# Kernel optimization log

Measured on AMD Instinct MI355X. Metric: run time of the kernel, lower is better.

## Reference

```python
import jax, jax.numpy as jnp
import numpy as np

B, N, C = 8, 32768, 4
M = 11          # memory_length
D = 5           # degree
K = D * M       # basis size per (channel, time) = M linear + (D-1)*M envelope terms


def setup_inputs() -> dict:
    key = jax.random.key(0)
    kx, kw = jax.random.split(key)
    x = jax.random.normal(kx, (B, N, C, 2), dtype=jnp.float32)
    # xavier-uniform over [C, K]
    limit = float(np.sqrt(6.0 / (C + K)))
    Weight = jax.random.uniform(kw, (C, K), minval=-limit, maxval=limit, dtype=jnp.float32)
    return {"x": x, "Weight": Weight}


def _windows(a, m):
    # a: [..., L] -> [..., L-m+1, m]; windows[..., n, j] = a[..., n+j]
    n_out = a.shape[-1] - m + 1
    return jnp.stack([a[..., j:j + n_out] for j in range(m)], axis=-1)


def reference(x, Weight):
    b, n, c, _ = x.shape
    # [B,N,C,2] -> complex [B,C,N]
    xc = (x[..., 0] + 1j * x[..., 1]).transpose(0, 2, 1)
    pad = jnp.zeros((b, c, M - 1), dtype=xc.dtype)
    padded = jnp.concatenate([pad, xc], axis=2)                 # [B,C,N+M-1]
    windows_x = _windows(padded, M)                             # [B,C,N,M] complex
    amp = jnp.abs(padded)                                       # [B,C,N+M-1]
    x_degree = jnp.stack([amp ** i for i in range(1, D)], axis=1)  # [B,D-1,C,L]
    windows_degree = _windows(x_degree, M)                      # [B,D-1,C,N,M]
    mul_term = windows_x[:, None] * windows_degree              # [B,D-1,C,N,M] complex
    mul_term = mul_term.transpose(0, 2, 3, 1, 4).reshape(b, c, n, (D - 1) * M)
    x_input = jnp.concatenate([windows_x, mul_term], axis=3)    # [B,C,N,D*M]
    out_c = jnp.einsum('bcnk,ck->bcn', x_input, Weight.astype(x_input.dtype))
    out_c = out_c.transpose(0, 2, 1)                            # [B,N,C]
    return jnp.stack([out_c.real, out_c.imag], axis=3)          # [B,N,C,2]
```

## Files before the change

### kernel.cpp

```cpp
#include <hip/hip_runtime.h>

#define BB 8
#define NN 32768
#define CC 4
#define MM 11
#define DD 5
#define KK 55
#define BLOCK_N 256
#define HALO (MM - 1)
#define SS (BLOCK_N + HALO)


__global__ __launch_bounds__(256, 4)
void gmp_kernel(const float* __restrict__ x,
                const float* __restrict__ W,
                float* __restrict__ out) {
    __shared__ float4 smem[SS * 3];

    const int tid = threadIdx.x;
    const int b = blockIdx.y;
    const int n0 = blockIdx.x * BLOCK_N;

    const float4* xg = (const float4*)x + (size_t)b * NN * 2;

    for (int s = tid; s < SS; s += BLOCK_N) {
        const int t = n0 - HALO + s;
        float4 lo = make_float4(0.f, 0.f, 0.f, 0.f);
        float4 hi = lo;
        if (t >= 0) {
            lo = xg[2 * t];
            hi = xg[2 * t + 1];
        }
        float4 a;
        a.x = sqrtf(fmaf(lo.x, lo.x, lo.y * lo.y));
        a.y = sqrtf(fmaf(lo.z, lo.z, lo.w * lo.w));
        a.z = sqrtf(fmaf(hi.x, hi.x, hi.y * hi.y));
        a.w = sqrtf(fmaf(hi.z, hi.z, hi.w * hi.w));
        smem[s * 3 + 0] = lo;
        smem[s * 3 + 1] = hi;
        smem[s * 3 + 2] = a;
    }
    __syncthreads();

    float acc_re[CC] = {0.f, 0.f, 0.f, 0.f};
    float acc_im[CC] = {0.f, 0.f, 0.f, 0.f};

    #pragma unroll
    for (int j = 0; j < MM; j++) {
        const int s = tid + j;
        const float4 lo = smem[s * 3 + 0];
        const float4 hi = smem[s * 3 + 1];
        const float4 a  = smem[s * 3 + 2];
        const float re[CC] = {lo.x, lo.z, hi.x, hi.z};
        const float im[CC] = {lo.y, lo.w, hi.y, hi.w};
        const float am[CC] = {a.x, a.y, a.z, a.w};
        #pragma unroll
        for (int c = 0; c < CC; c++) {
            float p = W[c * KK + 4 * MM + j];
            p = fmaf(p, am[c], W[c * KK + 3 * MM + j]);
            p = fmaf(p, am[c], W[c * KK + 2 * MM + j]);
            p = fmaf(p, am[c], W[c * KK + 1 * MM + j]);
            p = fmaf(p, am[c], W[c * KK + 0 * MM + j]);
            acc_re[c] = fmaf(re[c], p, acc_re[c]);
            acc_im[c] = fmaf(im[c], p, acc_im[c]);
        }
    }

    const int n = n0 + tid;
    float4* og = (float4*)out + (size_t)(b * NN + n) * 2;
    og[0] = make_float4(acc_re[0], acc_im[0], acc_re[1], acc_im[1]);
    og[1] = make_float4(acc_re[2], acc_im[2], acc_re[3], acc_im[3]);
}

extern "C" void kernel_launch(void* const* d_in, const int* in_sizes, int n_in,
                              void* d_out, int out_size, void* d_ws, size_t ws_size,
                              hipStream_t stream) {
    const float* x = (const float*)d_in[0];
    const float* W = (const float*)d_in[1];
    float* out = (float*)d_out;

    dim3 grid(NN / BLOCK_N, BB);
    gmp_kernel<<<grid, BLOCK_N, 0, stream>>>(x, W, out);
}
```

Measured before the change: 63.51 us.

## Split channel pairs across grid z-dimension to increase parallelism and occupancy

```diff
diff --git a/kernel.cpp b/kernel.cpp
--- a/kernel.cpp
+++ b/kernel.cpp
@@ -4,72 +4,71 @@
 #define NN 32768
 #define CC 4
 #define MM 11
-#define DD 5
 #define KK 55
-#define BLOCK_N 256
+#define THREADS 256
 #define HALO (MM - 1)
-#define SS (BLOCK_N + HALO)
+#define SS (THREADS + HALO)
 
 
-__global__ __launch_bounds__(256, 4)
+__global__ __launch_bounds__(THREADS, 8)
 void gmp_kernel(const float* __restrict__ x,
                 const float* __restrict__ W,
                 float* __restrict__ out) {
-    __shared__ float4 smem[SS * 3];
+    __shared__ float4 zs[SS];
+    __shared__ float2 as2[SS];
 
     const int tid = threadIdx.x;
-    const int b = blockIdx.y;
-    const int n0 = blockIdx.x * BLOCK_N;
+    const int b  = blockIdx.y;
+    const int h  = blockIdx.z;
+    const int n0 = blockIdx.x * THREADS;
 
     const float4* xg = (const float4*)x + (size_t)b * NN * 2;
 
-    for (int s = tid; s < SS; s += BLOCK_N) {
+    for (int s = tid; s < SS; s += THREADS) {
         const int t = n0 - HALO + s;
-        float4 lo = make_float4(0.f, 0.f, 0.f, 0.f);
-        float4 hi = lo;
-        if (t >= 0) {
-            lo = xg[2 * t];
-            hi = xg[2 * t + 1];
-        }
-        float4 a;
-        a.x = sqrtf(fmaf(lo.x, lo.x, lo.y * lo.y));
-        a.y = sqrtf(fmaf(lo.z, lo.z, lo.w * lo.w));
-        a.z = sqrtf(fmaf(hi.x, hi.x, hi.y * hi.y));
-        a.w = sqrtf(fmaf(hi.z, hi.z, hi.w * hi.w));
-        smem[s * 3 + 0] = lo;
-        smem[s * 3 + 1] = hi;
-        smem[s * 3 + 2] = a;
+        float4 v = make_float4(0.f, 0.f, 0.f, 0.f);
+        if (t >= 0) v = xg[2 * t + h];
+        float2 a;
+        a.x = sqrtf(fmaf(v.x, v.x, v.y * v.y));
+        a.y = sqrtf(fmaf(v.z, v.z, v.w * v.w));
+        zs[s] = v;
+        as2[s] = a;
     }
     __syncthreads();
 
-    float acc_re[CC] = {0.f, 0.f, 0.f, 0.f};
-    float acc_im[CC] = {0.f, 0.f, 0.f, 0.f};
+    const float* W0 = W + (2 * h) * KK;
+    const float* W1 = W + (2 * h + 1) * KK;
+
+    float ar0 = 0.f, ai0 = 0.f, ar1 = 0.f, ai1 = 0.f;
 
     #pragma unroll
     for (int j = 0; j < MM; j++) {
         const int s = tid + j;
-        const float4 lo = smem[s * 3 + 0];
-        const float4 hi = smem[s * 3 + 1];
-        const float4 a  = smem[s * 3 + 2];
-        const float re[CC] = {lo.x, lo.z, hi.x, hi.z};
-        const float im[CC] = {lo.y, lo.w, hi.y, hi.w};
-        const float am[CC] = {a.x, a.y, a.z, a.w};
-        #pragma unroll
-        for (int c = 0; c < CC; c++) {
-            float p = W[c * KK + 4 * MM + j];
-            p = fmaf(p, am[c], W[c * KK + 3 * MM + j]);
-            p = fmaf(p, am[c], W[c * KK + 2 * MM + j]);
-            p = fmaf(p, am[c], W[c * KK + 1 * MM + j]);
-            p = fmaf(p, am[c], W[c * KK + 0 * MM + j]);
-            acc_re[c] = fmaf(re[c], p, acc_re[c]);
-            acc_im[c] = fmaf(im[c], p, acc_im[c]);
+        const float4 v = zs[s];
+        const float2 a = as2[s];
+        {
+            float p = W0[4 * MM + j];
+            p = fmaf(p, a.x, W0[3 * MM + j]);
+            p = fmaf(p, a.x, W0[2 * MM + j]);
+            p = fmaf(p, a.x, W0[1 * MM + j]);
+            p = fmaf(p, a.x, W0[0 * MM + j]);
+            ar0 = fmaf(v.x, p, ar0);
+            ai0 = fmaf(v.y, p, ai0);
+        }
+        {
+            float p = W1[4 * MM + j];
+            p = fmaf(p, a.y, W1[3 * MM + j]);
+            p = fmaf(p, a.y, W1[2 * MM + j]);
+            p = fmaf(p, a.y, W1[1 * MM + j]);
+            p = fmaf(p, a.y, W1[0 * MM + j]);
+            ar1 = fmaf(v.z, p, ar1);
+            ai1 = fmaf(v.w, p, ai1);
         }
     }
 
     const int n = n0 + tid;
-    float4* og = (float4*)out + (size_t)(b * NN + n) * 2;
-    og[0] = make_float4(acc_re[0], acc_im[0], acc_re[1], acc_im[1]);
-    og[1] = make_float4(acc_re[2], acc_im[2], acc_re[3], acc_im[3]);
+    float4* og = (float4*)out + ((size_t)(b * NN + n) * 2 + h);
+    *og = make_float4(ar0, ai0, ar1, ai1);
 }
 
 extern "C" void kernel_launch(void* const* d_in, const int* in_sizes, int n_in,
@@ -79,6 +78,6 @@
     const float* W = (const float*)d_in[1];
     float* out = (float*)d_out;
 
-    dim3 grid(NN / BLOCK_N, BB);
-    gmp_kernel<<<grid, BLOCK_N, 0, stream>>>(x, W, out);
+    dim3 grid(NN / THREADS, BB, 2);
+    gmp_kernel<<<grid, THREADS, 0, stream>>>(x, W, out);
 }
```

Result: no change. 62.53 us, median of 2 (-1.6%).
